# Kernel tuning notes

Measured on AMD Instinct MI355X. Metric: run time of the kernel, lower is better.

## Reference

```python
import jax, jax.numpy as jnp
import numpy as np

N_NODES = 50000
N_EDGES = 800000
F_IN = 128
HEADS = 2
F_OUT = 128  # out_channels == nfeat for the residual


def setup_inputs() -> dict:
    key = jax.random.key(0)
    k_x, k_e, k_u, k_c, k_w, k_b = jax.random.split(key, 6)
    x = jax.random.normal(k_x, (N_NODES, F_IN), dtype=jnp.float32)
    edge_index = jax.random.randint(k_e, (2, N_EDGES), 0, N_NODES, dtype=jnp.int64)
    # FeaStConv params (PyG init: normal(mean=0, std=0.1))
    u = 0.1 * jax.random.normal(k_u, (F_IN, HEADS), dtype=jnp.float32)       # attention proj
    c = 0.1 * jax.random.normal(k_c, (HEADS,), dtype=jnp.float32)            # attention bias
    w = 0.1 * jax.random.normal(k_w, (F_IN, HEADS * F_OUT), dtype=jnp.float32)  # lin weight
    bias = 0.1 * jax.random.normal(k_b, (F_OUT,), dtype=jnp.float32)
    return {"x": x, "edge_index": edge_index, "u": u, "c": c, "w": w, "bias": bias}


def _feast_conv(x, edge_index, u, c, w, bias):
    n = x.shape[0]
    # add self loops (PyG FeaStConv default add_self_loops=True)
    loops = jnp.arange(n, dtype=edge_index.dtype)
    src = jnp.concatenate([edge_index[0], loops])  # j (source / message sender)
    dst = jnp.concatenate([edge_index[1], loops])  # i (target / aggregator)
    e = src.shape[0]
    # per-edge attention over heads: q = softmax(u^T (x_j - x_i) + c)
    xi = x[dst]                                   # [E, F_in]
    xj = x[src]                                   # [E, F_in]
    q = jax.nn.softmax((xj - xi) @ u + c, axis=-1)  # [E, H]
    # per-node linear, then gather per edge
    xw = (x @ w).reshape(n, HEADS, F_OUT)         # [N, H, F_out]
    msg = jnp.einsum('eh,ehf->ef', q, xw[src])    # [E, F_out]
    # mean aggregation at destinations
    agg = jax.ops.segment_sum(msg, dst, num_segments=n)
    cnt = jax.ops.segment_sum(jnp.ones((e,), x.dtype), dst, num_segments=n)
    return agg / jnp.maximum(cnt, 1.0)[:, None] + bias


def reference(x, edge_index, u, c, w, bias):
    # module forward: x + relu(FeaStConv(x, edge_index))
    return x + jax.nn.relu(_feast_conv(x, edge_index, u, c, w, bias))
```

## Files before the change

### kernel.cpp

```cpp
#include <hip/hip_runtime.h>
#include <hip/hip_bf16.h>

constexpr int N_NODES = 50000;
constexpr int N_EDGES = 800000;
constexpr int F_IN    = 128;
constexpr int F_OUT   = 128;
constexpr int HEADS   = 2;
constexpr int WCOLS   = HEADS * F_OUT;
constexpr int WE_ROWS = 272;
constexpr int SEG     = 64;

typedef __attribute__((ext_vector_type(8))) short  bf16x8;
typedef __attribute__((ext_vector_type(4))) float  f32x4;
typedef __attribute__((ext_vector_type(2))) float  f32x2;

static __device__ __forceinline__ unsigned short f32_to_bf16_bits(float f) {
    unsigned int u = __float_as_uint(f);
    u += 0x7fffu + ((u >> 16) & 1u);
    return (unsigned short)(u >> 16);
}

__global__ __launch_bounds__(256) void wt_cnt_kernel(const float* __restrict__ w,
                                                     const float* __restrict__ u,
                                                     unsigned short* __restrict__ wTe,
                                                     int* __restrict__ cnt) {
    const int tid = blockIdx.x * 256 + threadIdx.x;
    if (tid < WE_ROWS * F_IN) {
        const int r = tid >> 7;
        const int k = tid & 127;
        float v;
        if (r < WCOLS)            v = w[k * WCOLS + r];
        else if (r < WCOLS + 2)   v = u[k * HEADS + (r - WCOLS)];
        else                      v = 0.f;
        wTe[tid] = f32_to_bf16_bits(v);
    }
    if (tid < N_NODES) cnt[tid] = 0;
}

constexpr int RG = 4;

__global__ __launch_bounds__(256) void proj_kernel(const float* __restrict__ x,
                                                   const unsigned short* __restrict__ wTe,
                                                   unsigned char* __restrict__ xwf,
                                                   float2* __restrict__ s_tab) {
    const int lane = threadIdx.x & 63;
    const int wv   = threadIdx.x >> 6;
    const int n0   = blockIdx.x * (16 * RG);
    const int l15  = lane & 15;
    const int kg   = lane >> 4;

    f32x4 acc[RG][4];
    f32x4 acc4[RG];
#pragma unroll
    for (int rg = 0; rg < RG; ++rg) {
        acc4[rg] = (f32x4){0.f, 0.f, 0.f, 0.f};
#pragma unroll
        for (int t = 0; t < 4; ++t) acc[rg][t] = acc4[rg];
    }

#pragma unroll
    for (int ks = 0; ks < 4; ++ks) {
        bf16x8 xf[RG];
#pragma unroll
        for (int rg = 0; rg < RG; ++rg) {
            const int row = min(n0 + rg * 16 + l15, N_NODES - 1);
            const float* xp = x + (size_t)row * F_IN + ks * 32 + kg * 8;
            const float4 xa = *(const float4*)xp;
            const float4 xb = *(const float4*)(xp + 4);
            xf[rg][0] = (short)f32_to_bf16_bits(xa.x);
            xf[rg][1] = (short)f32_to_bf16_bits(xa.y);
            xf[rg][2] = (short)f32_to_bf16_bits(xa.z);
            xf[rg][3] = (short)f32_to_bf16_bits(xa.w);
            xf[rg][4] = (short)f32_to_bf16_bits(xb.x);
            xf[rg][5] = (short)f32_to_bf16_bits(xb.y);
            xf[rg][6] = (short)f32_to_bf16_bits(xb.z);
            xf[rg][7] = (short)f32_to_bf16_bits(xb.w);
        }

        const unsigned short* wbase = wTe + (size_t)(wv * 64 + l15) * F_IN + ks * 32 + kg * 8;
        const bf16x8 wf0 = *(const bf16x8*)(wbase);
        const bf16x8 wf1 = *(const bf16x8*)(wbase + 16 * F_IN);
        const bf16x8 wf2 = *(const bf16x8*)(wbase + 32 * F_IN);
        const bf16x8 wf3 = *(const bf16x8*)(wbase + 48 * F_IN);

#pragma unroll
        for (int rg = 0; rg < RG; ++rg) {
            acc[rg][0] = __builtin_amdgcn_mfma_f32_16x16x32_bf16(wf0, xf[rg], acc[rg][0], 0, 0, 0);
            acc[rg][1] = __builtin_amdgcn_mfma_f32_16x16x32_bf16(wf1, xf[rg], acc[rg][1], 0, 0, 0);
            acc[rg][2] = __builtin_amdgcn_mfma_f32_16x16x32_bf16(wf2, xf[rg], acc[rg][2], 0, 0, 0);
            acc[rg][3] = __builtin_amdgcn_mfma_f32_16x16x32_bf16(wf3, xf[rg], acc[rg][3], 0, 0, 0);
        }
        if (wv == 3) {
            const unsigned short* ubase = wTe + (size_t)(256 + l15) * F_IN + ks * 32 + kg * 8;
            const bf16x8 uf = *(const bf16x8*)(ubase);
#pragma unroll
            for (int rg = 0; rg < RG; ++rg)
                acc4[rg] = __builtin_amdgcn_mfma_f32_16x16x32_bf16(uf, xf[rg], acc4[rg], 0, 0, 0);
        }
    }

#pragma unroll
    for (int rg = 0; rg < RG; ++rg) {
        const int row = n0 + rg * 16 + l15;
        if (row < N_NODES) {
            unsigned char* orow = xwf + (size_t)row * WCOLS + wv * 64 + kg * 4;
#pragma unroll
            for (int t = 0; t < 4; ++t) {
                unsigned int pk = 0;
                pk = __builtin_amdgcn_cvt_pk_fp8_f32(acc[rg][t][0], acc[rg][t][1], pk, false);
                pk = __builtin_amdgcn_cvt_pk_fp8_f32(acc[rg][t][2], acc[rg][t][3], pk, true);
                *(unsigned int*)(orow + t * 16) = pk;
            }
            if (wv == 3 && kg == 0) {
                s_tab[row] = make_float2(acc4[rg][0], acc4[rg][1]);
            }
        }
    }
}

constexpr int EPT    = 4;
constexpr int CHUNK  = 256 * EPT;
constexpr int NCHUNK = (N_EDGES + CHUNK - 1) / CHUNK;
constexpr int NGROUP = 8;
constexpr int DRANGE = N_NODES / NGROUP;

__global__ __launch_bounds__(256) void scatter_kernel(const int* __restrict__ ei,
                                                      const float2* __restrict__ s,
                                                      const float* __restrict__ c,
                                                      int* __restrict__ cnt,
                                                      unsigned int* __restrict__ rec) {
    const int g     = blockIdx.x & (NGROUP - 1);
    const int chunk = blockIdx.x >> 3;
    const int dlo   = g * DRANGE;
    const int dhi   = dlo + DRANGE;
    const int base  = chunk * CHUNK + threadIdx.x;
    const float c0 = c[0], c1 = c[1];

    int  dstv[EPT];
    bool keep[EPT];
#pragma unroll
    for (int k = 0; k < EPT; ++k) {
        const int e = base + k * 256;
        const int ec = (e < N_EDGES) ? e : 0;
        dstv[k] = ei[N_EDGES + ec];
        keep[k] = (e < N_EDGES) && (dstv[k] >= dlo) && (dstv[k] < dhi);
    }
    int pos[EPT], srcv[EPT];
#pragma unroll
    for (int k = 0; k < EPT; ++k) {
        pos[k]  = keep[k] ? atomicAdd(&cnt[dstv[k]], 1) : 0;
        const int e = base + k * 256;
        srcv[k] = keep[k] ? ei[e] : 0;
    }
#pragma unroll
    for (int k = 0; k < EPT; ++k) {
        if (keep[k]) {
            const float2 ss = s[srcv[k]];
            const float2 sd = s[dstv[k]];
            const float l0 = ss.x - sd.x + c0;
            const float l1 = ss.y - sd.y + c1;
            const float m  = fmaxf(l0, l1);
            const float e0 = __expf(l0 - m);
            const float e1 = __expf(l1 - m);
            const float q0 = e0 / (e0 + e1);
            const unsigned int q16 = (unsigned int)(q0 * 65535.0f + 0.5f);
            const int p = min(pos[k], SEG - 1);
            rec[(size_t)dstv[k] * SEG + p] = (q16 << 16) | (unsigned int)srcv[k];
        }
    }
}

#define AGG_SLOT(K, A)                                                        \
    {                                                                         \
        const unsigned int r = rp[j + K];                                     \
        const unsigned int g = *(const unsigned int*)(gb + (size_t)(r & 0xffffu) * WCOLS); \
        const float q = fmaf(qsign, (float)(r >> 16) * (1.0f/65535.0f), qbase);\
        const f32x2 glo = __builtin_amdgcn_cvt_pk_f32_fp8(g, false);          \
        const f32x2 ghi = __builtin_amdgcn_cvt_pk_f32_fp8(g, true);           \
        A.x = fmaf(q, glo[0], A.x);                                           \
        A.y = fmaf(q, glo[1], A.y);                                           \
        A.z = fmaf(q, ghi[0], A.z);                                           \
        A.w = fmaf(q, ghi[1], A.w);                                           \
    }

__global__ __launch_bounds__(256) void agg_kernel(const float* __restrict__ x,
                                                  const float* __restrict__ bias,
                                                  const float* __restrict__ c,
                                                  const unsigned char* __restrict__ xwf,
                                                  const unsigned int* __restrict__ rec,
                                                  const int* __restrict__ cnt,
                                                  float* __restrict__ out) {
    const int lane = threadIdx.x & 63;
    const int half = lane >> 5;
    const int l5   = lane & 31;
    const int n    = blockIdx.x * 4 + (threadIdx.x >> 6);
    if (n >= N_NODES) return;
    const int m_cnt = min(cnt[n], SEG);
    const int deg   = m_cnt + 1;
    const unsigned int* rp = rec + (size_t)n * SEG;

    const float qbase = half ? 1.0f : 0.0f;
    const float qsign = half ? -1.0f : 1.0f;
    const unsigned char* gb = xwf + half * F_OUT + 4 * l5;

    const float c0 = c[0], c1 = c[1];
    const float mm = fmaxf(c0, c1);
    const float se0 = __expf(c0 - mm);
    const float se1 = __expf(c1 - mm);
    const float qs = fmaf(qsign, se0 / (se0 + se1), qbase);
    const unsigned int gsv = *(const unsigned int*)(gb + (size_t)n * WCOLS);
    const f32x2 slo = __builtin_amdgcn_cvt_pk_f32_fp8(gsv, false);
    const f32x2 shi = __builtin_amdgcn_cvt_pk_f32_fp8(gsv, true);
    float4 a0, a1 = {0.f,0.f,0.f,0.f}, a2 = a1, a3 = a1;
    a0.x = qs * slo[0];
    a0.y = qs * slo[1];
    a0.z = qs * shi[0];
    a0.w = qs * shi[1];

    int j = 0;
    for (; j + 4 <= m_cnt; j += 4) {
        AGG_SLOT(0, a0) AGG_SLOT(1, a1) AGG_SLOT(2, a2) AGG_SLOT(3, a3)
    }
    for (; j < m_cnt; ++j) {
        AGG_SLOT(0, a0)
    }
    float4 t;
    t.x = (a0.x + a1.x) + (a2.x + a3.x);
    t.y = (a0.y + a1.y) + (a2.y + a3.y);
    t.z = (a0.z + a1.z) + (a2.z + a3.z);
    t.w = (a0.w + a1.w) + (a2.w + a3.w);
    t.x += __shfl_xor(t.x, 32, 64);
    t.y += __shfl_xor(t.y, 32, 64);
    t.z += __shfl_xor(t.z, 32, 64);
    t.w += __shfl_xor(t.w, 32, 64);
    if (half == 0) {
        const float inv = 1.0f / (float)deg;
        const float4 bv = *(const float4*)(bias + 4 * l5);
        const float4 xv = *(const float4*)(x + (size_t)n * F_IN + 4 * l5);
        float4 r;
        r.x = xv.x + fmaxf(fmaf(t.x, inv, bv.x), 0.f);
        r.y = xv.y + fmaxf(fmaf(t.y, inv, bv.y), 0.f);
        r.z = xv.z + fmaxf(fmaf(t.z, inv, bv.z), 0.f);
        r.w = xv.w + fmaxf(fmaf(t.w, inv, bv.w), 0.f);
        *(float4*)(out + (size_t)n * F_OUT + 4 * l5) = r;
    }
}

extern "C" void kernel_launch(void* const* d_in, const int* in_sizes, int n_in,
                              void* d_out, int out_size, void* d_ws, size_t ws_size,
                              hipStream_t stream) {
    const float* x    = (const float*)d_in[0];
    const int*   ei   = (const int*)  d_in[1];
    const float* u    = (const float*)d_in[2];
    const float* c    = (const float*)d_in[3];
    const float* w    = (const float*)d_in[4];
    const float* bias = (const float*)d_in[5];
    float* out = (float*)d_out;

    char* p = (char*)d_ws;
    unsigned char* xwf = (unsigned char*)p;    p += (size_t)N_NODES * WCOLS;
    float2* s_tab  = (float2*)p;               p += (size_t)N_NODES * sizeof(float2);
    int*    cnt    = (int*)p;                  p += (size_t)N_NODES * sizeof(int);
    unsigned short* wTe = (unsigned short*)p;  p += (size_t)WE_ROWS * F_IN * sizeof(unsigned short);
    unsigned int* rec = (unsigned int*)p;

    wt_cnt_kernel<<<(N_NODES + 255) / 256, 256, 0, stream>>>(w, u, wTe, cnt);

    proj_kernel<<<(N_NODES + 16 * RG - 1) / (16 * RG), 256, 0, stream>>>(x, wTe, xwf, s_tab);

    scatter_kernel<<<NGROUP * NCHUNK, 256, 0, stream>>>(ei, s_tab, c, cnt, rec);

    agg_kernel<<<(N_NODES + 3) / 4, 256, 0, stream>>>(x, bias, c, xwf, rec, cnt, out);
}
```

Measured before the change: 123.6 us.

## Add nontemporal loads/stores, vectorize record reads, remap agg blocks to dst groups

```diff
diff --git a/kernel.cpp b/kernel.cpp
--- a/kernel.cpp
+++ b/kernel.cpp
@@ -13,6 +13,7 @@
 typedef __attribute__((ext_vector_type(8))) short  bf16x8;
 typedef __attribute__((ext_vector_type(4))) float  f32x4;
 typedef __attribute__((ext_vector_type(2))) float  f32x2;
+typedef __attribute__((ext_vector_type(4))) unsigned int u32x4;
 
 static __device__ __forceinline__ unsigned short f32_to_bf16_bits(float f) {
     unsigned int u = __float_as_uint(f);
@@ -65,16 +66,16 @@
         for (int rg = 0; rg < RG; ++rg) {
             const int row = min(n0 + rg * 16 + l15, N_NODES - 1);
             const float* xp = x + (size_t)row * F_IN + ks * 32 + kg * 8;
-            const float4 xa = *(const float4*)xp;
-            const float4 xb = *(const float4*)(xp + 4);
-            xf[rg][0] = (short)f32_to_bf16_bits(xa.x);
-            xf[rg][1] = (short)f32_to_bf16_bits(xa.y);
-            xf[rg][2] = (short)f32_to_bf16_bits(xa.z);
-            xf[rg][3] = (short)f32_to_bf16_bits(xa.w);
-            xf[rg][4] = (short)f32_to_bf16_bits(xb.x);
-            xf[rg][5] = (short)f32_to_bf16_bits(xb.y);
-            xf[rg][6] = (short)f32_to_bf16_bits(xb.z);
-            xf[rg][7] = (short)f32_to_bf16_bits(xb.w);
+            const f32x4 xa = __builtin_nontemporal_load((const f32x4*)xp);
+            const f32x4 xb = __builtin_nontemporal_load((const f32x4*)(xp + 4));
+            xf[rg][0] = (short)f32_to_bf16_bits(xa[0]);
+            xf[rg][1] = (short)f32_to_bf16_bits(xa[1]);
+            xf[rg][2] = (short)f32_to_bf16_bits(xa[2]);
+            xf[rg][3] = (short)f32_to_bf16_bits(xa[3]);
+            xf[rg][4] = (short)f32_to_bf16_bits(xb[0]);
+            xf[rg][5] = (short)f32_to_bf16_bits(xb[1]);
+            xf[rg][6] = (short)f32_to_bf16_bits(xb[2]);
+            xf[rg][7] = (short)f32_to_bf16_bits(xb[3]);
         }
 
         const unsigned short* wbase = wTe + (size_t)(wv * 64 + l15) * F_IN + ks * 32 + kg * 8;
@@ -142,7 +143,7 @@
     for (int k = 0; k < EPT; ++k) {
         const int e = base + k * 256;
         const int ec = (e < N_EDGES) ? e : 0;
-        dstv[k] = ei[N_EDGES + ec];
+        dstv[k] = __builtin_nontemporal_load(ei + N_EDGES + ec);
         keep[k] = (e < N_EDGES) && (dstv[k] >= dlo) && (dstv[k] < dhi);
     }
     int pos[EPT], srcv[EPT];
@@ -150,7 +151,7 @@
     for (int k = 0; k < EPT; ++k) {
         pos[k]  = keep[k] ? atomicAdd(&cnt[dstv[k]], 1) : 0;
         const int e = base + k * 256;
-        srcv[k] = keep[k] ? ei[e] : 0;
+        srcv[k] = keep[k] ? __builtin_nontemporal_load(ei + e) : 0;
     }
 #pragma unroll
     for (int k = 0; k < EPT; ++k) {
@@ -170,9 +171,9 @@
     }
 }
 
-#define AGG_SLOT(K, A)                                                        \
+#define AGG_GATHER(RV, A)                                                     \
     {                                                                         \
-        const unsigned int r = rp[j + K];                                     \
+        const unsigned int r = (RV);                                          \
         const unsigned int g = *(const unsigned int*)(gb + (size_t)(r & 0xffffu) * WCOLS); \
         const float q = fmaf(qsign, (float)(r >> 16) * (1.0f/65535.0f), qbase);\
         const f32x2 glo = __builtin_amdgcn_cvt_pk_f32_fp8(g, false);          \
@@ -182,6 +183,8 @@
         A.z = fmaf(q, ghi[0], A.z);                                           \
         A.w = fmaf(q, ghi[1], A.w);                                           \
     }
+
+constexpr int AGG_GPB = (DRANGE + 3) / 4;
 
 __global__ __launch_bounds__(256) void agg_kernel(const float* __restrict__ x,
                                                   const float* __restrict__ bias,
@@ -193,8 +196,10 @@
     const int lane = threadIdx.x & 63;
     const int half = lane >> 5;
     const int l5   = lane & 31;
-    const int n    = blockIdx.x * 4 + (threadIdx.x >> 6);
-    if (n >= N_NODES) return;
+    const int g    = blockIdx.x & (NGROUP - 1);
+    const int nloc = (blockIdx.x >> 3) * 4 + (threadIdx.x >> 6);
+    if (nloc >= DRANGE) return;
+    const int n = g * DRANGE + nloc;
     const int m_cnt = min(cnt[n], SEG);
     const int deg   = m_cnt + 1;
     const unsigned int* rp = rec + (size_t)n * SEG;
@@ -219,10 +224,12 @@
 
     int j = 0;
     for (; j + 4 <= m_cnt; j += 4) {
-        AGG_SLOT(0, a0) AGG_SLOT(1, a1) AGG_SLOT(2, a2) AGG_SLOT(3, a3)
+        const u32x4 r4 = *(const u32x4*)(rp + j);
+        AGG_GATHER(r4[0], a0) AGG_GATHER(r4[1], a1)
+        AGG_GATHER(r4[2], a2) AGG_GATHER(r4[3], a3)
     }
     for (; j < m_cnt; ++j) {
-        AGG_SLOT(0, a0)
+        AGG_GATHER(rp[j], a0)
     }
     float4 t;
     t.x = (a0.x + a1.x) + (a2.x + a3.x);
@@ -236,13 +243,13 @@
     if (half == 0) {
         const float inv = 1.0f / (float)deg;
         const float4 bv = *(const float4*)(bias + 4 * l5);
-        const float4 xv = *(const float4*)(x + (size_t)n * F_IN + 4 * l5);
-        float4 r;
-        r.x = xv.x + fmaxf(fmaf(t.x, inv, bv.x), 0.f);
-        r.y = xv.y + fmaxf(fmaf(t.y, inv, bv.y), 0.f);
-        r.z = xv.z + fmaxf(fmaf(t.z, inv, bv.z), 0.f);
-        r.w = xv.w + fmaxf(fmaf(t.w, inv, bv.w), 0.f);
-        *(float4*)(out + (size_t)n * F_OUT + 4 * l5) = r;
+        const f32x4 xv = __builtin_nontemporal_load((const f32x4*)(x + (size_t)n * F_IN + 4 * l5));
+        f32x4 r;
+        r[0] = xv[0] + fmaxf(fmaf(t.x, inv, bv.x), 0.f);
+        r[1] = xv[1] + fmaxf(fmaf(t.y, inv, bv.y), 0.f);
+        r[2] = xv[2] + fmaxf(fmaf(t.z, inv, bv.z), 0.f);
+        r[3] = xv[3] + fmaxf(fmaf(t.w, inv, bv.w), 0.f);
+        __builtin_nontemporal_store(r, (f32x4*)(out + (size_t)n * F_OUT + 4 * l5));
     }
 }
 
@@ -270,5 +277,5 @@
 
     scatter_kernel<<<NGROUP * NCHUNK, 256, 0, stream>>>(ei, s_tab, c, cnt, rec);
 
-    agg_kernel<<<(N_NODES + 3) / 4, 256, 0, stream>>>(x, bias, c, xwf, rec, cnt, out);
-}
+    agg_kernel<<<NGROUP * AGG_GPB, 256, 0, stream>>>(x, bias, c, xwf, rec, cnt, out);
+}
```

New measurement: 143.5 us. 1.16x slower.
